# Kernel tuning notes

Measured on AMD Instinct MI355X. Metric: run time of the kernel, lower is better.

The kernel has to match this reference:

```python
import jax, jax.numpy as jnp
import numpy as np

N_NODES = 50000
N_EDGES = 800000
D_FEAT = 128


def setup_inputs() -> dict:
    key = jax.random.key(0)
    k1, k2, k3, k4 = jax.random.split(key, 4)
    node_att = jax.random.normal(k1, (N_NODES, D_FEAT), dtype=jnp.float32)
    edge_att = jax.random.normal(k2, (N_EDGES, D_FEAT), dtype=jnp.float32)
    src = jax.random.randint(k3, (N_EDGES,), 0, N_NODES, dtype=jnp.int64)
    dst = jax.random.randint(k4, (N_EDGES,), 0, N_NODES, dtype=jnp.int64)
    return {"node_att": node_att, "edge_att": edge_att, "src": src, "dst": dst}


def reference(node_att, edge_att, src, dst):
    # update_all: message = edge_att * src_att; reduce = sum over incoming
    # edges (segment-sum keyed by dst) + own att, then softmax over features.
    msg = edge_att * node_att[src]                     # [E, d]
    agg = jax.ops.segment_sum(msg, dst, num_segments=node_att.shape[0])  # [N, d]
    new_node_att = jax.nn.softmax(agg + node_att, axis=1)  # [N, d]

    # apply_edges (uses UPDATED node atts): src*dst + edge_att, softmax over features.
    prob = new_node_att[src] * new_node_att[dst] + edge_att  # [E, d]
    new_edge_att = jax.nn.softmax(prob, axis=1)
    return new_node_att, new_edge_att
```

## Files before the change

kernel.cpp:

```cpp
#include <hip/hip_runtime.h>

#define NFEAT 128
#define CAP   64

typedef float v4f __attribute__((ext_vector_type(4)));

__device__ __forceinline__ v4f nt_load4(const float* p) {
    return __builtin_nontemporal_load(reinterpret_cast<const v4f*>(p));
}
__device__ __forceinline__ v4f ld4(const float* p) {
    return *reinterpret_cast<const v4f*>(p);
}
__device__ __forceinline__ void nt_store4(float* p, v4f v) {
    __builtin_nontemporal_store(v, reinterpret_cast<v4f*>(p));
}

__global__ void zero_kernel(int* __restrict__ p, int n) {
    int i = blockIdx.x * blockDim.x + threadIdx.x;
    if (i < n) p[i] = 0;
}

__global__ void bucket_fill_kernel(const int* __restrict__ dst,
                                   const int* __restrict__ src,
                                   int* __restrict__ counts,
                                   int2* __restrict__ bucket, int n_edges) {
    int e = blockIdx.x * blockDim.x + threadIdx.x;
    if (e < n_edges) {
        int d = dst[e];
        int s = src[e];
        int pos = atomicAdd(&counts[d], 1);
        if (pos < CAP)
            bucket[(size_t)d * CAP + pos] = make_int2(e, s);
    }
}

__global__ void node_gather_softmax_kernel(const float* __restrict__ node_att,
                                           const float* __restrict__ edge_att,
                                           const int2* __restrict__ bucket,
                                           const int* __restrict__ counts,
                                           float* __restrict__ out, int n_nodes) {
    int t = blockIdx.x * blockDim.x + threadIdx.x;
    int r = t >> 5;
    int lane = t & 31;
    int c = lane << 2;
    if (r >= n_nodes) return;

    size_t base = (size_t)r * NFEAT + c;
    v4f acc = ld4(node_att + base);

    int cnt = min(counts[r], CAP);
    size_t bbase = (size_t)r * CAP;

    for (int tbase = 0; tbase < cnt; tbase += 32) {
        int li = tbase + lane;
        int e_l = 0, s_l = 0;
        if (li < cnt) {
            int2 p = bucket[bbase + li];
            e_l = p.x; s_l = p.y;
        }
        int m = min(32, cnt - tbase);
        #pragma unroll 8
        for (int j = 0; j < m; ++j) {
            int e = __shfl(e_l, j, 32);
            int s = __shfl(s_l, j, 32);
            v4f ea = nt_load4(edge_att + (size_t)e * NFEAT + c);
            v4f na = ld4(node_att + (size_t)s * NFEAT + c);
            acc += ea * na;
        }
    }

    float m4 = fmaxf(fmaxf(acc.x, acc.y), fmaxf(acc.z, acc.w));
    #pragma unroll
    for (int off = 16; off > 0; off >>= 1)
        m4 = fmaxf(m4, __shfl_xor(m4, off, 32));

    acc.x = __expf(acc.x - m4); acc.y = __expf(acc.y - m4);
    acc.z = __expf(acc.z - m4); acc.w = __expf(acc.w - m4);

    float s = acc.x + acc.y + acc.z + acc.w;
    #pragma unroll
    for (int off = 16; off > 0; off >>= 1)
        s += __shfl_xor(s, off, 32);

    float inv = 1.0f / s;
    acc *= inv;
    *reinterpret_cast<v4f*>(out + base) = acc;
}

__global__ void edge_softmax_kernel(const float* __restrict__ new_node,
                                    const float* __restrict__ edge_att,
                                    const int* __restrict__ src,
                                    const int* __restrict__ dst,
                                    float* __restrict__ out, int n_edges) {
    int t = blockIdx.x * blockDim.x + threadIdx.x;
    int e = t >> 5;
    int c = (t & 31) << 2;
    if (e >= n_edges) return;

    int s_i = src[e];
    int d_i = dst[e];

    v4f ns = ld4(new_node + (size_t)s_i * NFEAT + c);
    v4f nd = ld4(new_node + (size_t)d_i * NFEAT + c);
    v4f ea = nt_load4(edge_att + (size_t)e * NFEAT + c);

    v4f v = ns * nd + ea;

    float m = fmaxf(fmaxf(v.x, v.y), fmaxf(v.z, v.w));
    #pragma unroll
    for (int off = 16; off > 0; off >>= 1)
        m = fmaxf(m, __shfl_xor(m, off, 32));

    v.x = __expf(v.x - m); v.y = __expf(v.y - m);
    v.z = __expf(v.z - m); v.w = __expf(v.w - m);

    float s = v.x + v.y + v.z + v.w;
    #pragma unroll
    for (int off = 16; off > 0; off >>= 1)
        s += __shfl_xor(s, off, 32);

    float inv = 1.0f / s;
    v *= inv;
    nt_store4(out + (size_t)e * NFEAT + c, v);
}

extern "C" void kernel_launch(void* const* d_in, const int* in_sizes, int n_in,
                              void* d_out, int out_size, void* d_ws, size_t ws_size,
                              hipStream_t stream) {
    const float* node_att = (const float*)d_in[0];
    const float* edge_att = (const float*)d_in[1];
    const int*   src      = (const int*)d_in[2];
    const int*   dst      = (const int*)d_in[3];

    int n_nodes = in_sizes[0] / NFEAT;
    int n_edges = in_sizes[2];

    float* out_node = (float*)d_out;
    float* out_edge = out_node + (size_t)n_nodes * NFEAT;

    int2* bucket = (int2*)d_ws;
    int*  counts = (int*)(bucket + (size_t)n_nodes * CAP);

    const int BLK = 256;

    {
        int grid = (n_nodes + BLK - 1) / BLK;
        zero_kernel<<<grid, BLK, 0, stream>>>(counts, n_nodes);
    }
    {
        int grid = (n_edges + BLK - 1) / BLK;
        bucket_fill_kernel<<<grid, BLK, 0, stream>>>(dst, src, counts,
                                                     bucket, n_edges);
    }
    {
        long long threads = (long long)n_nodes * 32;
        int grid = (int)((threads + BLK - 1) / BLK);
        node_gather_softmax_kernel<<<grid, BLK, 0, stream>>>(
            node_att, edge_att, bucket, counts, out_node, n_nodes);
    }
    {
        long long threads = (long long)n_edges * 32;
        int grid = (int)((threads + BLK - 1) / BLK);
        edge_softmax_kernel<<<grid, BLK, 0, stream>>>(
            out_node, edge_att, src, dst, out_edge, n_edges);
    }
}
```

Baseline: 385.9 us.

## Process edge softmax per destination node via buckets to reuse dst row

Replaces the per-edge softmax kernel with a per-destination-node kernel that walks the dst bucket built earlier, loading the destination node row once and looping over its incoming edges. This removes the dst index read and the repeated loads of the dst row. In exchange parallelism drops to one 32-lane group per node with a serial edge loop, which reduces memory-level parallelism. Edges beyond the bucket capacity would be silently skipped.

```diff
diff --git a/kernel.cpp b/kernel.cpp
--- a/kernel.cpp
+++ b/kernel.cpp
@@ -87,41 +87,56 @@
     *reinterpret_cast<v4f*>(out + base) = acc;
 }
 
-__global__ void edge_softmax_kernel(const float* __restrict__ new_node,
-                                    const float* __restrict__ edge_att,
-                                    const int* __restrict__ src,
-                                    const int* __restrict__ dst,
-                                    float* __restrict__ out, int n_edges) {
+__global__ void edge_softmax_bucket_kernel(const float* __restrict__ new_node,
+                                           const float* __restrict__ edge_att,
+                                           const int2* __restrict__ bucket,
+                                           const int* __restrict__ counts,
+                                           float* __restrict__ out, int n_nodes) {
     int t = blockIdx.x * blockDim.x + threadIdx.x;
-    int e = t >> 5;
-    int c = (t & 31) << 2;
-    if (e >= n_edges) return;
+    int r = t >> 5;
+    int lane = t & 31;
+    int c = lane << 2;
+    if (r >= n_nodes) return;
 
-    int s_i = src[e];
-    int d_i = dst[e];
+    int cnt = min(counts[r], CAP);
+    if (cnt == 0) return;
 
-    v4f ns = ld4(new_node + (size_t)s_i * NFEAT + c);
-    v4f nd = ld4(new_node + (size_t)d_i * NFEAT + c);
-    v4f ea = nt_load4(edge_att + (size_t)e * NFEAT + c);
+    v4f nd = ld4(new_node + (size_t)r * NFEAT + c);
+    size_t bbase = (size_t)r * CAP;
 
-    v4f v = ns * nd + ea;
+    for (int tbase = 0; tbase < cnt; tbase += 32) {
+        int li = tbase + lane;
+        int e_l = 0, s_l = 0;
+        if (li < cnt) {
+            int2 p = bucket[bbase + li];
+            e_l = p.x; s_l = p.y;
+        }
+        int m = min(32, cnt - tbase);
+        for (int j = 0; j < m; ++j) {
+            int e = __shfl(e_l, j, 32);
+            int s = __shfl(s_l, j, 32);
+            v4f ns = ld4(new_node + (size_t)s * NFEAT + c);
+            v4f ea = nt_load4(edge_att + (size_t)e * NFEAT + c);
 
-    float m = fmaxf(fmaxf(v.x, v.y), fmaxf(v.z, v.w));
-    #pragma unroll
-    for (int off = 16; off > 0; off >>= 1)
-        m = fmaxf(m, __shfl_xor(m, off, 32));
+            v4f v = ns * nd + ea;
 
-    v.x = __expf(v.x - m); v.y = __expf(v.y - m);
-    v.z = __expf(v.z - m); v.w = __expf(v.w - m);
+            float mm = fmaxf(fmaxf(v.x, v.y), fmaxf(v.z, v.w));
+            #pragma unroll
+            for (int off = 16; off > 0; off >>= 1)
+                mm = fmaxf(mm, __shfl_xor(mm, off, 32));
 
-    float s = v.x + v.y + v.z + v.w;
-    #pragma unroll
-    for (int off = 16; off > 0; off >>= 1)
-        s += __shfl_xor(s, off, 32);
+            v.x = __expf(v.x - mm); v.y = __expf(v.y - mm);
+            v.z = __expf(v.z - mm); v.w = __expf(v.w - mm);
 
-    float inv = 1.0f / s;
-    v *= inv;
-    nt_store4(out + (size_t)e * NFEAT + c, v);
+            float ss = v.x + v.y + v.z + v.w;
+            #pragma unroll
+            for (int off = 16; off > 0; off >>= 1)
+                ss += __shfl_xor(ss, off, 32);
+
+            v *= (1.0f / ss);
+            nt_store4(out + (size_t)e * NFEAT + c, v);
+        }
+    }
 }
 
 extern "C" void kernel_launch(void* const* d_in, const int* in_sizes, int n_in,
@@ -159,9 +174,9 @@
             node_att, edge_att, bucket, counts, out_node, n_nodes);
     }
     {
-        long long threads = (long long)n_edges * 32;
+        long long threads = (long long)n_nodes * 32;
         int grid = (int)((threads + BLK - 1) / BLK);
-        edge_softmax_kernel<<<grid, BLK, 0, stream>>>(
-            out_node, edge_att, src, dst, out_edge, n_edges);
+        edge_softmax_bucket_kernel<<<grid, BLK, 0, stream>>>(
+            out_node, edge_att, bucket, counts, out_edge, n_nodes);
     }
 }
```

Measured after the change: 371.9 us, median of 2. -3.6%, faster.
